# Performance work log

Hardware: AMD Instinct MI355X
Metric: run time of the kernel (lower is better)

The kernel has to match this reference:

```python
import jax, jax.numpy as jnp
import numpy as np


def _graph_conv(src, dst, x, num_nodes, inv_sqrt_out, inv_sqrt_in):
    # DGL GraphConv, norm='both': h = D_in^{-1/2} A D_out^{-1/2} x
    msg = (x * inv_sqrt_out[:, None])[src]                      # [E, F] gather
    agg = jax.ops.segment_sum(msg, dst, num_segments=num_nodes)  # [N, F] scatter-add
    return agg * inv_sqrt_in[:, None]


def setup_inputs() -> dict:
    key = jax.random.key(0)
    ks = jax.random.split(key, 8)
    N, E, IN, H, C = 4096, 131072, 512, 8192, 16
    return {
        "features": jax.random.normal(ks[0], (N, IN), dtype=jnp.float32),
        "W1": jax.random.normal(ks[1], (IN, H), dtype=jnp.float32) * 0.02,
        "b1": jnp.zeros((H,), dtype=jnp.float32),
        "W2": jax.random.normal(ks[2], (H, N), dtype=jnp.float32) * 0.02,
        "Wl": jax.random.normal(ks[3], (N, C), dtype=jnp.float32) * 0.02,
        "bl": jnp.zeros((C,), dtype=jnp.float32),
        "src": jax.random.randint(ks[4], (E,), 0, N, dtype=jnp.int32),
        "dst": jax.random.randint(ks[5], (E,), 0, N, dtype=jnp.int32),
    }


def reference(features, W1, b1, W2, Wl, bl, src, dst):
    N = features.shape[0]
    ones = jnp.ones(src.shape, dtype=features.dtype)
    deg_out = jnp.clip(jax.ops.segment_sum(ones, src, num_segments=N), 1.0)
    deg_in = jnp.clip(jax.ops.segment_sum(ones, dst, num_segments=N), 1.0)
    inv_sqrt_out = jax.lax.rsqrt(deg_out)
    inv_sqrt_in = jax.lax.rsqrt(deg_in)

    # conv1: project then aggregate (math identical to DGL's ordering)
    x = features @ W1 + b1
    x = _graph_conv(src, dst, x, N, inv_sqrt_out, inv_sqrt_in)   # [N, 2N]
    # dropout: identity in inference mode
    # conv2 (weight passed externally, no bias)
    x = x @ W2
    x = _graph_conv(src, dst, x, N, inv_sqrt_out, inv_sqrt_in)   # [N, N]
    x = jax.nn.relu(x)
    x = x @ Wl + bl                                              # [N, C]
    return jax.nn.softmax(x, axis=1)
```

## Files before the change

### kernel.cpp

```cpp
#include <hip/hip_runtime.h>
#include <cstdint>
#include <cstddef>


using bf8   = __attribute__((ext_vector_type(8))) short;
using s4    = __attribute__((ext_vector_type(4))) short;
using f32x4 = __attribute__((ext_vector_type(4))) float;

static __device__ __forceinline__ unsigned short f2bf(float f) {
    union { float f; uint32_t u; } v; v.f = f;
    uint32_t r = (v.u + 0x7FFFu + ((v.u >> 16) & 1u)) >> 16;
    return (unsigned short)r;
}
static __device__ __forceinline__ float bf2f(unsigned short b) {
    union { uint32_t u; float f; } v; v.u = ((uint32_t)b) << 16;
    return v.f;
}

static __device__ __forceinline__ void gload16(const short* g, short* l) {
    __builtin_amdgcn_global_load_lds(
        (const __attribute__((address_space(1))) unsigned int*)g,
        (__attribute__((address_space(3))) unsigned int*)l,
        16, 0, 0);
}


__global__ void k_zero(float* a, float* b, int* c, int n) {
    int i = blockIdx.x * blockDim.x + threadIdx.x;
    if (i < n) { a[i] = 0.f; b[i] = 0.f; c[i] = 0; }
}

__global__ void k_count(const int* __restrict__ src, const int* __restrict__ dst,
                        float* deg_out, float* deg_in, int E) {
    int e = blockIdx.x * blockDim.x + threadIdx.x;
    if (e < E) {
        atomicAdd(&deg_out[src[e]], 1.f);
        atomicAdd(&deg_in[dst[e]], 1.f);
    }
}

__global__ void k_inv(const float* deg_out, const float* deg_in,
                      float* inv_out, float* inv_in, int n) {
    int i = blockIdx.x * blockDim.x + threadIdx.x;
    if (i < n) {
        inv_out[i] = rsqrtf(fmaxf(deg_out[i], 1.f));
        inv_in[i]  = rsqrtf(fmaxf(deg_in[i], 1.f));
    }
}

__global__ void k_scan(const float* __restrict__ deg_in, int* __restrict__ row_off) {
    __shared__ int part[1024];
    const int t = threadIdx.x;
    int v0 = (int)deg_in[t*4+0], v1 = (int)deg_in[t*4+1],
        v2 = (int)deg_in[t*4+2], v3 = (int)deg_in[t*4+3];
    part[t] = v0 + v1 + v2 + v3;
    __syncthreads();
    for (int off = 1; off < 1024; off <<= 1) {
        int x = (t >= off) ? part[t - off] : 0;
        __syncthreads();
        part[t] += x;
        __syncthreads();
    }
    int run = (t == 0) ? 0 : part[t-1];
    row_off[t*4+0] = run; run += v0;
    row_off[t*4+1] = run; run += v1;
    row_off[t*4+2] = run; run += v2;
    row_off[t*4+3] = run; run += v3;
    if (t == 1023) row_off[4096] = run;
}

__global__ void k_fill(const int* __restrict__ src, const int* __restrict__ dst,
                       const int* __restrict__ row_off, int* cursor,
                       int* __restrict__ esrc, int E) {
    int e = blockIdx.x * blockDim.x + threadIdx.x;
    if (e < E) {
        int d = dst[e];
        int p = atomicAdd(&cursor[d], 1);
        esrc[row_off[d] + p] = src[e];
    }
}

__global__ void k_rowsum(const int* __restrict__ row_off, const int* __restrict__ esrc,
                         const float* __restrict__ inv_out, const float* __restrict__ inv_in,
                         float* __restrict__ rowsum) {
    const int node = blockIdx.x, lane = threadIdx.x;
    const int beg = row_off[node], end = row_off[node + 1];
    float s = 0.f;
    for (int p = beg + lane; p < end; p += 64) s += inv_out[esrc[p]];
    #pragma unroll
    for (int off = 32; off; off >>= 1) s += __shfl_down(s, off, 64);
    if (lane == 0) rowsum[node] = s * inv_in[node];
}

__global__ void k_cvt_scale(const float* __restrict__ in, const float* __restrict__ sc,
                            short* __restrict__ out, int n4, int f4) {
    int i = blockIdx.x * blockDim.x + threadIdx.x;
    if (i < n4) {
        const float s = sc[i / f4];
        float4 v = reinterpret_cast<const float4*>(in)[i];
        s4 o;
        o[0] = (short)f2bf(v.x * s); o[1] = (short)f2bf(v.y * s);
        o[2] = (short)f2bf(v.z * s); o[3] = (short)f2bf(v.w * s);
        reinterpret_cast<s4*>(out)[i] = o;
    }
}

__global__ void k_tr2(const float* __restrict__ in, short* __restrict__ out, int R, int C) {
    __shared__ float tile[64][33];
    const int bc = blockIdx.x * 32, br = blockIdx.y * 64;
    const int tx = threadIdx.x, ty = threadIdx.y;
    #pragma unroll
    for (int dy = 0; dy < 64; dy += 8)
        tile[ty + dy][tx] = in[(size_t)(br + ty + dy) * C + bc + tx];
    __syncthreads();
    #pragma unroll
    for (int dy = 0; dy < 32; dy += 8) {
        const int oy = ty + dy;
        ushort2 o;
        o.x = f2bf(tile[tx * 2][oy]);
        o.y = f2bf(tile[tx * 2 + 1][oy]);
        *reinterpret_cast<ushort2*>(&out[(size_t)(bc + oy) * R + br + tx * 2]) = o;
    }
}

template<int EPI>
__global__ __launch_bounds__(512, 2)
void gemm8p(const short* __restrict__ A, const short* __restrict__ Bt,
            short* __restrict__ C,
            const float* __restrict__ bias, const float* __restrict__ rs,
            int M, int N, int K)
{
    constexpr int USZ  = 4096;
    constexpr int BOFF = 4 * USZ;
    constexpr int BUF  = 8 * USZ;
    __shared__ __align__(16) short lds[2 * BUF];
    const int tid  = threadIdx.x;
    const int wid  = tid >> 6, lane = tid & 63;
    const int wm   = wid >> 2;
    const int wn   = wid & 3;
    const int fr   = lane & 15;
    const int kq   = lane >> 4;
    const int nt   = K >> 6;

    const int gx  = gridDim.x;
    const int nwg = gx * gridDim.y;
    int bid = blockIdx.y * gx + blockIdx.x;
    bid = (bid & 7) * (nwg >> 3) + (bid >> 3);
    const int tm = (bid / gx) * 256;
    const int tn = (bid % gx) * 256;

    const int srow = tid >> 3;
    const int scq  = tid & 7;
    const int scs  = scq ^ (srow & 7);
    const short* gA = A  + (size_t)(tm + srow) * K + scs * 8;
    const short* gB = Bt + (size_t)(tn + srow) * K + scs * 8;
    short* const ldst = lds + tid * 8;

    const int cx0 = (0 * 4 + kq) ^ (fr & 7);
    const int cx1 = (1 * 4 + kq) ^ (fr & 7);
    int aoff[8][2], boff[4][2];
    #pragma unroll
    for (int mi = 0; mi < 8; ++mi) {
        const int r = wm * 128 + mi * 16 + fr;
        aoff[mi][0] = r * 64 + cx0 * 8;
        aoff[mi][1] = r * 64 + cx1 * 8;
    }
    #pragma unroll
    for (int n = 0; n < 4; ++n) {
        const int r = wn * 64 + n * 16 + fr;
        boff[n][0] = BOFF + r * 64 + cx0 * 8;
        boff[n][1] = BOFF + r * 64 + cx1 * 8;
    }

    f32x4 acc[8][4];
    #pragma unroll
    for (int mi = 0; mi < 8; ++mi)
        #pragma unroll
        for (int n = 0; n < 4; ++n)
            acc[mi][n] = (f32x4){0.f, 0.f, 0.f, 0.f};

    #pragma unroll
    for (int u = 0; u < 4; ++u) gload16(gA + (size_t)u * 64 * K, ldst + u * USZ);
    #pragma unroll
    for (int v = 0; v < 4; ++v) gload16(gB + (size_t)v * 64 * K, ldst + BOFF + v * USZ);
    #pragma unroll
    for (int u = 0; u < 4; ++u) gload16(gA + (size_t)u * 64 * K + 64, ldst + BUF + u * USZ);
    #pragma unroll
    for (int v = 0; v < 4; ++v) gload16(gB + (size_t)v * 64 * K + 64, ldst + BUF + BOFF + v * USZ);
    asm volatile("s_waitcnt vmcnt(8)" ::: "memory");
    __builtin_amdgcn_sched_barrier(0);
    __builtin_amdgcn_s_barrier();

    for (int t = 0; t < nt; ++t) {
        const int cc = (t & 1) * BUF;
        const bool pf = (t + 2 < nt);
        const size_t kf = (size_t)(t + 2) * 64;

        bf8 a03[4][2], a47[4][2], bg[4][2];

        #pragma unroll
        for (int mi = 0; mi < 4; ++mi)
            #pragma unroll
            for (int s = 0; s < 2; ++s)
                a03[mi][s] = *reinterpret_cast<const bf8*>(lds + cc + aoff[mi][s]);
        #pragma unroll
        for (int n = 0; n < 2; ++n)
            #pragma unroll
            for (int s = 0; s < 2; ++s)
                bg[n][s] = *reinterpret_cast<const bf8*>(lds + cc + boff[n][s]);
        __builtin_amdgcn_s_barrier();
        asm volatile("s_waitcnt lgkmcnt(0)" ::: "memory");
        __builtin_amdgcn_sched_barrier(0);
        __builtin_amdgcn_s_setprio(1);
        #pragma unroll
        for (int mi = 0; mi < 4; ++mi)
            #pragma unroll
            for (int n = 0; n < 2; ++n)
                #pragma unroll
                for (int s = 0; s < 2; ++s)
                    acc[mi][n] = __builtin_amdgcn_mfma_f32_16x16x32_bf16(a03[mi][s], bg[n][s], acc[mi][n], 0, 0, 0);
        __builtin_amdgcn_s_setprio(0);
        __builtin_amdgcn_s_barrier();

        #pragma unroll
        for (int n = 2; n < 4; ++n)
            #pragma unroll
            for (int s = 0; s < 2; ++s)
                bg[n][s] = *reinterpret_cast<const bf8*>(lds + cc + boff[n][s]);
        __builtin_amdgcn_s_barrier();
        asm volatile("s_waitcnt lgkmcnt(0)" ::: "memory");
        __builtin_amdgcn_sched_barrier(0);
        __builtin_amdgcn_s_setprio(1);
        #pragma unroll
        for (int mi = 0; mi < 4; ++mi)
            #pragma unroll
            for (int n = 2; n < 4; ++n)
                #pragma unroll
                for (int s = 0; s < 2; ++s)
                    acc[mi][n] = __builtin_amdgcn_mfma_f32_16x16x32_bf16(a03[mi][s], bg[n][s], acc[mi][n], 0, 0, 0);
        __builtin_amdgcn_s_setprio(0);
        __builtin_amdgcn_s_barrier();

        #pragma unroll
        for (int mi = 0; mi < 4; ++mi)
            #pragma unroll
            for (int s = 0; s < 2; ++s)
                a47[mi][s] = *reinterpret_cast<const bf8*>(lds + cc + aoff[4 + mi][s]);
        if (pf) {
            #pragma unroll
            for (int v = 0; v < 4; ++v)
                gload16(gB + (size_t)v * 64 * K + kf, ldst + cc + BOFF + v * USZ);
        }
        __builtin_amdgcn_s_barrier();
        asm volatile("s_waitcnt lgkmcnt(0)" ::: "memory");
        __builtin_amdgcn_sched_barrier(0);
        __builtin_amdgcn_s_setprio(1);
        #pragma unroll
        for (int mi = 0; mi < 4; ++mi)
            #pragma unroll
            for (int n = 0; n < 2; ++n)
                #pragma unroll
                for (int s = 0; s < 2; ++s)
                    acc[4 + mi][n] = __builtin_amdgcn_mfma_f32_16x16x32_bf16(a47[mi][s], bg[n][s], acc[4 + mi][n], 0, 0, 0);
        __builtin_amdgcn_s_setprio(0);
        __builtin_amdgcn_s_barrier();

        if (pf) {
            #pragma unroll
            for (int u = 0; u < 4; ++u)
                gload16(gA + (size_t)u * 64 * K + kf, ldst + cc + u * USZ);
        }
        __builtin_amdgcn_s_setprio(1);
        #pragma unroll
        for (int mi = 0; mi < 4; ++mi)
            #pragma unroll
            for (int n = 2; n < 4; ++n)
                #pragma unroll
                for (int s = 0; s < 2; ++s)
                    acc[4 + mi][n] = __builtin_amdgcn_mfma_f32_16x16x32_bf16(a47[mi][s], bg[n][s], acc[4 + mi][n], 0, 0, 0);
        __builtin_amdgcn_s_setprio(0);
        if (pf) {
            asm volatile("s_waitcnt vmcnt(8)" ::: "memory");
        } else if (t + 2 == nt) {
            asm volatile("s_waitcnt vmcnt(0)" ::: "memory");
        }
        __builtin_amdgcn_sched_barrier(0);
        __builtin_amdgcn_s_barrier();
    }

    const int rb = kq * 4;
    #pragma unroll
    for (int mi = 0; mi < 8; ++mi) {
        #pragma unroll
        for (int n = 0; n < 4; ++n) {
            const int col = tn + wn * 64 + n * 16 + fr;
            const float bcol = (EPI == 1) ? bias[col] : 0.f;
            #pragma unroll
            for (int j = 0; j < 4; ++j) {
                const int row = tm + wm * 128 + mi * 16 + rb + j;
                float v = acc[mi][n][j];
                if (EPI == 1) v += rs[row] * bcol;
                else          v *= rs[row];
                C[(size_t)row * N + col] = (short)f2bf(v);
            }
        }
    }
}

template<int RELU>
__global__ __launch_bounds__(64)
void agg_strip(const short* __restrict__ X, short* __restrict__ Y,
               const int* __restrict__ row_off, const int* __restrict__ esrc,
               const float* __restrict__ inv_in, int F)
{
    const int node = blockIdx.y;
    const int c0 = blockIdx.x * 512 + threadIdx.x * 8;
    float acc[8];
    #pragma unroll
    for (int j = 0; j < 8; ++j) acc[j] = 0.f;

    const int beg = row_off[node], end = row_off[node + 1];
    int p = beg;
    for (; p + 3 < end; p += 4) {
        const int s0 = esrc[p], s1 = esrc[p + 1], s2 = esrc[p + 2], s3 = esrc[p + 3];
        bf8 x0 = *reinterpret_cast<const bf8*>(X + (size_t)s0 * F + c0);
        bf8 x1 = *reinterpret_cast<const bf8*>(X + (size_t)s1 * F + c0);
        bf8 x2 = *reinterpret_cast<const bf8*>(X + (size_t)s2 * F + c0);
        bf8 x3 = *reinterpret_cast<const bf8*>(X + (size_t)s3 * F + c0);
        #pragma unroll
        for (int j = 0; j < 8; ++j)
            acc[j] += (bf2f((unsigned short)x0[j]) + bf2f((unsigned short)x1[j]))
                    + (bf2f((unsigned short)x2[j]) + bf2f((unsigned short)x3[j]));
    }
    for (; p < end; ++p) {
        const int s0 = esrc[p];
        bf8 x0 = *reinterpret_cast<const bf8*>(X + (size_t)s0 * F + c0);
        #pragma unroll
        for (int j = 0; j < 8; ++j) acc[j] += bf2f((unsigned short)x0[j]);
    }
    const float sc = inv_in[node];
    bf8 o;
    #pragma unroll
    for (int j = 0; j < 8; ++j) {
        float v = acc[j] * sc;
        if (RELU) v = fmaxf(v, 0.f);
        o[j] = (short)f2bf(v);
    }
    *reinterpret_cast<bf8*>(Y + (size_t)node * F + c0) = o;
}

__global__ __launch_bounds__(256)
void k_head(const short* __restrict__ H, const float* __restrict__ Wl,
            const float* __restrict__ bl, float* __restrict__ out)
{
    const int row = blockIdx.x;
    const int tid = threadIdx.x;
    float acc[16];
    #pragma unroll
    for (int c = 0; c < 16; ++c) acc[c] = 0.f;

    for (int k = tid; k < 4096; k += 256) {
        const float x = bf2f((unsigned short)H[(size_t)row * 4096 + k]);
        const float4* w = reinterpret_cast<const float4*>(Wl + (size_t)k * 16);
        float4 w0 = w[0], w1 = w[1], w2 = w[2], w3 = w[3];
        acc[0]  += x * w0.x; acc[1]  += x * w0.y; acc[2]  += x * w0.z; acc[3]  += x * w0.w;
        acc[4]  += x * w1.x; acc[5]  += x * w1.y; acc[6]  += x * w1.z; acc[7]  += x * w1.w;
        acc[8]  += x * w2.x; acc[9]  += x * w2.y; acc[10] += x * w2.z; acc[11] += x * w2.w;
        acc[12] += x * w3.x; acc[13] += x * w3.y; acc[14] += x * w3.z; acc[15] += x * w3.w;
    }
    #pragma unroll
    for (int c = 0; c < 16; ++c)
        for (int off = 32; off; off >>= 1)
            acc[c] += __shfl_down(acc[c], off, 64);

    __shared__ float sm[16][4];
    const int wid = tid >> 6, lane = tid & 63;
    if (lane == 0) {
        #pragma unroll
        for (int c = 0; c < 16; ++c) sm[c][wid] = acc[c];
    }
    __syncthreads();
    if (tid < 16) {
        float l = sm[tid][0] + sm[tid][1] + sm[tid][2] + sm[tid][3] + bl[tid];
        float mx = l;
        #pragma unroll
        for (int off = 1; off < 16; off <<= 1) mx = fmaxf(mx, __shfl_xor(mx, off, 16));
        float e = expf(l - mx);
        float s = e;
        #pragma unroll
        for (int off = 1; off < 16; off <<= 1) s += __shfl_xor(s, off, 16);
        out[(size_t)row * 16 + tid] = e / s;
    }
}


extern "C" void kernel_launch(void* const* d_in, const int* in_sizes, int n_in,
                              void* d_out, int out_size, void* d_ws, size_t ws_size,
                              hipStream_t stream)
{
    const float* features = (const float*)d_in[0];
    const float* W1       = (const float*)d_in[1];
    const float* b1       = (const float*)d_in[2];
    const float* W2       = (const float*)d_in[3];
    const float* Wl       = (const float*)d_in[4];
    const float* bl       = (const float*)d_in[5];
    const int*   src      = (const int*)d_in[6];
    const int*   dst      = (const int*)d_in[7];
    float* out = (float*)d_out;

    const int N = 4096, IN = 512, H = 8192;
    const int E = in_sizes[6];

    char* ws = (char*)d_ws;
    size_t o = 0;
    auto alloc = [&](size_t bytes) -> char* {
        char* p = ws + o;
        o = (o + bytes + 255) & ~(size_t)255;
        return p;
    };
    short* W2t   = (short*)alloc((size_t)N * H * 2);
    short* h1    = (short*)alloc((size_t)N * H * 2);
    short* x2s   = (short*)alloc((size_t)N * N * 2);
    short* featb = (short*)alloc((size_t)N * IN * 2);
    short* aggF  = (short*)alloc((size_t)N * IN * 2);
    short* W1t   = (short*)alloc((size_t)H * IN * 2);
    float* deg_out = (float*)alloc(N * 4);
    float* deg_in  = (float*)alloc(N * 4);
    float* inv_out = (float*)alloc(N * 4);
    float* inv_in  = (float*)alloc(N * 4);
    float* rowsum  = (float*)alloc(N * 4);
    int*   cursor  = (int*)alloc(N * 4);
    int*   row_off = (int*)alloc((N + 1) * 4);
    int*   esrc    = (int*)alloc((size_t)E * 4);
    short* h2 = h1;

    k_zero <<<(N + 255) / 256, 256, 0, stream>>>(deg_out, deg_in, cursor, N);
    k_count<<<(E + 255) / 256, 256, 0, stream>>>(src, dst, deg_out, deg_in, E);
    k_inv  <<<(N + 255) / 256, 256, 0, stream>>>(deg_out, deg_in, inv_out, inv_in, N);
    k_scan <<<1, 1024, 0, stream>>>(deg_in, row_off);
    k_fill <<<(E + 255) / 256, 256, 0, stream>>>(src, dst, row_off, cursor, esrc, E);
    k_rowsum<<<N, 64, 0, stream>>>(row_off, esrc, inv_out, inv_in, rowsum);

    k_cvt_scale<<<(N * IN / 4 + 255) / 256, 256, 0, stream>>>(features, inv_out, featb,
                                                              N * IN / 4, IN / 4);
    k_tr2<<<dim3(H / 32, IN / 64), dim3(32, 8), 0, stream>>>(W1, W1t, IN, H);
    k_tr2<<<dim3(N / 32, H / 64), dim3(32, 8), 0, stream>>>(W2, W2t, H, N);

    agg_strip<0><<<dim3(1, N), 64, 0, stream>>>(featb, aggF, row_off, esrc, inv_in, IN);
    gemm8p<1><<<dim3(H / 256, N / 256), 512, 0, stream>>>(aggF, W1t, h1, b1, rowsum, N, H, IN);

    gemm8p<2><<<dim3(N / 256, N / 256), 512, 0, stream>>>(h1, W2t, x2s, nullptr, inv_out, N, N, H);
    agg_strip<1><<<dim3(N / 512, N), 64, 0, stream>>>(x2s, h2, row_off, esrc, inv_in, N);

    k_head<<<N, 256, 0, stream>>>(h2, Wl, bl, out);
}
```

Before: 476.0 us.

## Simplify GEMM main loop to single-phase load/compute with fewer barriers

Replaces the four-phase ping-pong main loop, which interleaved LDS reads, MFMA quadrants, setprio and global prefetches across several barriers, with one simpler loop per K-tile. Each iteration waits on vmcnt, takes one barrier, reads all A/B fragments per k-slice, issues all 32 MFMAs, then takes a second barrier and prefetches the tile two steps ahead. This cuts barrier count and scheduling complexity. In exchange it loses the fine-grained overlap of LDS reads and global loads with MFMA work, and the s_setprio wave prioritisation.

```diff
diff --git a/kernel.cpp b/kernel.cpp
--- a/kernel.cpp
+++ b/kernel.cpp
@@ -187,105 +187,43 @@
     for (int u = 0; u < 4; ++u) gload16(gA + (size_t)u * 64 * K + 64, ldst + BUF + u * USZ);
     #pragma unroll
     for (int v = 0; v < 4; ++v) gload16(gB + (size_t)v * 64 * K + 64, ldst + BUF + BOFF + v * USZ);
-    asm volatile("s_waitcnt vmcnt(8)" ::: "memory");
-    __builtin_amdgcn_sched_barrier(0);
-    __builtin_amdgcn_s_barrier();
 
     for (int t = 0; t < nt; ++t) {
         const int cc = (t & 1) * BUF;
-        const bool pf = (t + 2 < nt);
-        const size_t kf = (size_t)(t + 2) * 64;
-
-        bf8 a03[4][2], a47[4][2], bg[4][2];
-
-        #pragma unroll
-        for (int mi = 0; mi < 4; ++mi)
-            #pragma unroll
-            for (int s = 0; s < 2; ++s)
-                a03[mi][s] = *reinterpret_cast<const bf8*>(lds + cc + aoff[mi][s]);
-        #pragma unroll
-        for (int n = 0; n < 2; ++n)
-            #pragma unroll
-            for (int s = 0; s < 2; ++s)
-                bg[n][s] = *reinterpret_cast<const bf8*>(lds + cc + boff[n][s]);
+
+        if (t + 1 < nt) { asm volatile("s_waitcnt vmcnt(8)" ::: "memory"); }
+        else            { asm volatile("s_waitcnt vmcnt(0)" ::: "memory"); }
+        __builtin_amdgcn_sched_barrier(0);
         __builtin_amdgcn_s_barrier();
+
+        #pragma unroll
+        for (int s = 0; s < 2; ++s) {
+            bf8 b[4], a[8];
+            #pragma unroll
+            for (int n = 0; n < 4; ++n)
+                b[n] = *reinterpret_cast<const bf8*>(lds + cc + boff[n][s]);
+            #pragma unroll
+            for (int mi = 0; mi < 8; ++mi)
+                a[mi] = *reinterpret_cast<const bf8*>(lds + cc + aoff[mi][s]);
+            #pragma unroll
+            for (int mi = 0; mi < 8; ++mi)
+                #pragma unroll
+                for (int n = 0; n < 4; ++n)
+                    acc[mi][n] = __builtin_amdgcn_mfma_f32_16x16x32_bf16(a[mi], b[n], acc[mi][n], 0, 0, 0);
+        }
+
         asm volatile("s_waitcnt lgkmcnt(0)" ::: "memory");
         __builtin_amdgcn_sched_barrier(0);
-        __builtin_amdgcn_s_setprio(1);
-        #pragma unroll
-        for (int mi = 0; mi < 4; ++mi)
-            #pragma unroll
-            for (int n = 0; n < 2; ++n)
-                #pragma unroll
-                for (int s = 0; s < 2; ++s)
-                    acc[mi][n] = __builtin_amdgcn_mfma_f32_16x16x32_bf16(a03[mi][s], bg[n][s], acc[mi][n], 0, 0, 0);
-        __builtin_amdgcn_s_setprio(0);
         __builtin_amdgcn_s_barrier();
-
-        #pragma unroll
-        for (int n = 2; n < 4; ++n)
-            #pragma unroll
-            for (int s = 0; s < 2; ++s)
-                bg[n][s] = *reinterpret_cast<const bf8*>(lds + cc + boff[n][s]);
-        __builtin_amdgcn_s_barrier();
-        asm volatile("s_waitcnt lgkmcnt(0)" ::: "memory");
-        __builtin_amdgcn_sched_barrier(0);
-        __builtin_amdgcn_s_setprio(1);
-        #pragma unroll
-        for (int mi = 0; mi < 4; ++mi)
-            #pragma unroll
-            for (int n = 2; n < 4; ++n)
-                #pragma unroll
-                for (int s = 0; s < 2; ++s)
-                    acc[mi][n] = __builtin_amdgcn_mfma_f32_16x16x32_bf16(a03[mi][s], bg[n][s], acc[mi][n], 0, 0, 0);
-        __builtin_amdgcn_s_setprio(0);
-        __builtin_amdgcn_s_barrier();
-
-        #pragma unroll
-        for (int mi = 0; mi < 4; ++mi)
-            #pragma unroll
-            for (int s = 0; s < 2; ++s)
-                a47[mi][s] = *reinterpret_cast<const bf8*>(lds + cc + aoff[4 + mi][s]);
-        if (pf) {
+        if (t + 2 < nt) {
+            const size_t kf = (size_t)(t + 2) * 64;
+            #pragma unroll
+            for (int u = 0; u < 4; ++u)
+                gload16(gA + (size_t)u * 64 * K + kf, ldst + cc + u * USZ);
             #pragma unroll
             for (int v = 0; v < 4; ++v)
                 gload16(gB + (size_t)v * 64 * K + kf, ldst + cc + BOFF + v * USZ);
         }
-        __builtin_amdgcn_s_barrier();
-        asm volatile("s_waitcnt lgkmcnt(0)" ::: "memory");
-        __builtin_amdgcn_sched_barrier(0);
-        __builtin_amdgcn_s_setprio(1);
-        #pragma unroll
-        for (int mi = 0; mi < 4; ++mi)
-            #pragma unroll
-            for (int n = 0; n < 2; ++n)
-                #pragma unroll
-                for (int s = 0; s < 2; ++s)
-                    acc[4 + mi][n] = __builtin_amdgcn_mfma_f32_16x16x32_bf16(a47[mi][s], bg[n][s], acc[4 + mi][n], 0, 0, 0);
-        __builtin_amdgcn_s_setprio(0);
-        __builtin_amdgcn_s_barrier();
-
-        if (pf) {
-            #pragma unroll
-            for (int u = 0; u < 4; ++u)
-                gload16(gA + (size_t)u * 64 * K + kf, ldst + cc + u * USZ);
-        }
-        __builtin_amdgcn_s_setprio(1);
-        #pragma unroll
-        for (int mi = 0; mi < 4; ++mi)
-            #pragma unroll
-            for (int n = 2; n < 4; ++n)
-                #pragma unroll
-                for (int s = 0; s < 2; ++s)
-                    acc[4 + mi][n] = __builtin_amdgcn_mfma_f32_16x16x32_bf16(a47[mi][s], bg[n][s], acc[4 + mi][n], 0, 0, 0);
-        __builtin_amdgcn_s_setprio(0);
-        if (pf) {
-            asm volatile("s_waitcnt vmcnt(8)" ::: "memory");
-        } else if (t + 2 == nt) {
-            asm volatile("s_waitcnt vmcnt(0)" ::: "memory");
-        }
-        __builtin_amdgcn_sched_barrier(0);
-        __builtin_amdgcn_s_barrier();
     }
 
     const int rb = kq * 4;
```

After: 482.1 us. No clear change (+1.3%).

## Software-pipeline LDS fragment loads across K iterations in GEMM main loop

Applied to the files above, without the earlier changes.

Restructures the GEMM main loop so fragments for the next K-tile (aL, bL) are read from LDS during the current iteration's MFMA phases, rather than at the start of each iteration. It also removes the explicit lgkmcnt(0) waits and sched_barriers and splits the A global prefetch into two halves issued at different phases. The goal is to hide LDS read latency behind MFMAs and spread global-to-LDS traffic more evenly. In exchange it uses more registers, and correctness now depends on the reworked barrier and vmcnt ordering, since buffers are reused while next-tile reads are in flight.

```diff
diff --git a/kernel.cpp b/kernel.cpp
--- a/kernel.cpp
+++ b/kernel.cpp
@@ -179,6 +179,8 @@
         for (int n = 0; n < 4; ++n)
             acc[mi][n] = (f32x4){0.f, 0.f, 0.f, 0.f};
 
+    bf8 aL[4][2], aH[4][2], bL[2][2], bH[2][2];
+
     #pragma unroll
     for (int u = 0; u < 4; ++u) gload16(gA + (size_t)u * 64 * K, ldst + u * USZ);
     #pragma unroll
@@ -191,26 +193,49 @@
     __builtin_amdgcn_sched_barrier(0);
     __builtin_amdgcn_s_barrier();
 
+    #pragma unroll
+    for (int mi = 0; mi < 4; ++mi)
+        #pragma unroll
+        for (int s = 0; s < 2; ++s)
+            aL[mi][s] = *reinterpret_cast<const bf8*>(lds + aoff[mi][s]);
+    #pragma unroll
+    for (int n = 0; n < 2; ++n)
+        #pragma unroll
+        for (int s = 0; s < 2; ++s)
+            bL[n][s] = *reinterpret_cast<const bf8*>(lds + boff[n][s]);
+
     for (int t = 0; t < nt; ++t) {
         const int cc = (t & 1) * BUF;
+        const int cn = cc ^ BUF;
         const bool pf = (t + 2 < nt);
+        const bool nx = (t + 1 < nt);
         const size_t kf = (size_t)(t + 2) * 64;
 
-        bf8 a03[4][2], a47[4][2], bg[4][2];
-
+        if (!nx) { asm volatile("s_waitcnt vmcnt(0)" ::: "memory"); }
+
+        #pragma unroll
+        for (int n = 0; n < 2; ++n)
+            #pragma unroll
+            for (int s = 0; s < 2; ++s)
+                bH[n][s] = *reinterpret_cast<const bf8*>(lds + cc + boff[2 + n][s]);
+        __builtin_amdgcn_s_barrier();
+        __builtin_amdgcn_s_setprio(1);
         #pragma unroll
         for (int mi = 0; mi < 4; ++mi)
             #pragma unroll
+            for (int n = 0; n < 2; ++n)
+                #pragma unroll
+                for (int s = 0; s < 2; ++s)
+                    acc[mi][n] = __builtin_amdgcn_mfma_f32_16x16x32_bf16(aL[mi][s], bL[n][s], acc[mi][n], 0, 0, 0);
+        __builtin_amdgcn_s_setprio(0);
+        __builtin_amdgcn_s_barrier();
+
+        #pragma unroll
+        for (int mi = 0; mi < 4; ++mi)
+            #pragma unroll
             for (int s = 0; s < 2; ++s)
-                a03[mi][s] = *reinterpret_cast<const bf8*>(lds + cc + aoff[mi][s]);
-        #pragma unroll
-        for (int n = 0; n < 2; ++n)
-            #pragma unroll
-            for (int s = 0; s < 2; ++s)
-                bg[n][s] = *reinterpret_cast<const bf8*>(lds + cc + boff[n][s]);
-        __builtin_amdgcn_s_barrier();
-        asm volatile("s_waitcnt lgkmcnt(0)" ::: "memory");
-        __builtin_amdgcn_sched_barrier(0);
+                aH[mi][s] = *reinterpret_cast<const bf8*>(lds + cc + aoff[4 + mi][s]);
+        __builtin_amdgcn_s_barrier();
         __builtin_amdgcn_s_setprio(1);
         #pragma unroll
         for (int mi = 0; mi < 4; ++mi)
@@ -218,73 +243,60 @@
             for (int n = 0; n < 2; ++n)
                 #pragma unroll
                 for (int s = 0; s < 2; ++s)
-                    acc[mi][n] = __builtin_amdgcn_mfma_f32_16x16x32_bf16(a03[mi][s], bg[n][s], acc[mi][n], 0, 0, 0);
+                    acc[mi][2 + n] = __builtin_amdgcn_mfma_f32_16x16x32_bf16(aL[mi][s], bH[n][s], acc[mi][2 + n], 0, 0, 0);
         __builtin_amdgcn_s_setprio(0);
         __builtin_amdgcn_s_barrier();
 
-        #pragma unroll
-        for (int n = 2; n < 4; ++n)
-            #pragma unroll
-            for (int s = 0; s < 2; ++s)
-                bg[n][s] = *reinterpret_cast<const bf8*>(lds + cc + boff[n][s]);
-        __builtin_amdgcn_s_barrier();
-        asm volatile("s_waitcnt lgkmcnt(0)" ::: "memory");
-        __builtin_amdgcn_sched_barrier(0);
-        __builtin_amdgcn_s_setprio(1);
-        #pragma unroll
-        for (int mi = 0; mi < 4; ++mi)
-            #pragma unroll
-            for (int n = 2; n < 4; ++n)
-                #pragma unroll
-                for (int s = 0; s < 2; ++s)
-                    acc[mi][n] = __builtin_amdgcn_mfma_f32_16x16x32_bf16(a03[mi][s], bg[n][s], acc[mi][n], 0, 0, 0);
-        __builtin_amdgcn_s_setprio(0);
-        __builtin_amdgcn_s_barrier();
-
-        #pragma unroll
-        for (int mi = 0; mi < 4; ++mi)
-            #pragma unroll
-            for (int s = 0; s < 2; ++s)
-                a47[mi][s] = *reinterpret_cast<const bf8*>(lds + cc + aoff[4 + mi][s]);
         if (pf) {
             #pragma unroll
             for (int v = 0; v < 4; ++v)
                 gload16(gB + (size_t)v * 64 * K + kf, ldst + cc + BOFF + v * USZ);
-        }
-        __builtin_amdgcn_s_barrier();
-        asm volatile("s_waitcnt lgkmcnt(0)" ::: "memory");
-        __builtin_amdgcn_sched_barrier(0);
-        __builtin_amdgcn_s_setprio(1);
-        #pragma unroll
-        for (int mi = 0; mi < 4; ++mi)
-            #pragma unroll
-            for (int n = 0; n < 2; ++n)
-                #pragma unroll
-                for (int s = 0; s < 2; ++s)
-                    acc[4 + mi][n] = __builtin_amdgcn_mfma_f32_16x16x32_bf16(a47[mi][s], bg[n][s], acc[4 + mi][n], 0, 0, 0);
-        __builtin_amdgcn_s_setprio(0);
-        __builtin_amdgcn_s_barrier();
-
-        if (pf) {
-            #pragma unroll
-            for (int u = 0; u < 4; ++u)
-                gload16(gA + (size_t)u * 64 * K + kf, ldst + cc + u * USZ);
-        }
-        __builtin_amdgcn_s_setprio(1);
-        #pragma unroll
-        for (int mi = 0; mi < 4; ++mi)
-            #pragma unroll
-            for (int n = 2; n < 4; ++n)
-                #pragma unroll
-                for (int s = 0; s < 2; ++s)
-                    acc[4 + mi][n] = __builtin_amdgcn_mfma_f32_16x16x32_bf16(a47[mi][s], bg[n][s], acc[4 + mi][n], 0, 0, 0);
-        __builtin_amdgcn_s_setprio(0);
-        if (pf) {
-            asm volatile("s_waitcnt vmcnt(8)" ::: "memory");
-        } else if (t + 2 == nt) {
+            gload16(gA + (size_t)0 * 64 * K + kf, ldst + cc + 0 * USZ);
+            gload16(gA + (size_t)2 * 64 * K + kf, ldst + cc + 2 * USZ);
+            asm volatile("s_waitcnt vmcnt(6)" ::: "memory");
+        } else {
             asm volatile("s_waitcnt vmcnt(0)" ::: "memory");
         }
-        __builtin_amdgcn_sched_barrier(0);
+        if (nx) {
+            #pragma unroll
+            for (int mi = 0; mi < 4; ++mi)
+                #pragma unroll
+                for (int s = 0; s < 2; ++s)
+                    aL[mi][s] = *reinterpret_cast<const bf8*>(lds + cn + aoff[mi][s]);
+        }
+        __builtin_amdgcn_s_barrier();
+        __builtin_amdgcn_s_setprio(1);
+        #pragma unroll
+        for (int mi = 0; mi < 4; ++mi)
+            #pragma unroll
+            for (int n = 0; n < 2; ++n)
+                #pragma unroll
+                for (int s = 0; s < 2; ++s)
+                    acc[4 + mi][n] = __builtin_amdgcn_mfma_f32_16x16x32_bf16(aH[mi][s], bL[n][s], acc[4 + mi][n], 0, 0, 0);
+        __builtin_amdgcn_s_setprio(0);
+        __builtin_amdgcn_s_barrier();
+
+        if (pf) {
+            gload16(gA + (size_t)1 * 64 * K + kf, ldst + cc + 1 * USZ);
+            gload16(gA + (size_t)3 * 64 * K + kf, ldst + cc + 3 * USZ);
+        }
+        if (nx) {
+            #pragma unroll
+            for (int n = 0; n < 2; ++n)
+                #pragma unroll
+                for (int s = 0; s < 2; ++s)
+                    bL[n][s] = *reinterpret_cast<const bf8*>(lds + cn + boff[n][s]);
+        }
+        __builtin_amdgcn_s_barrier();
+        __builtin_amdgcn_s_setprio(1);
+        #pragma unroll
+        for (int mi = 0; mi < 4; ++mi)
+            #pragma unroll
+            for (int n = 0; n < 2; ++n)
+                #pragma unroll
+                for (int s = 0; s < 2; ++s)
+                    acc[4 + mi][2 + n] = __builtin_amdgcn_mfma_f32_16x16x32_bf16(aH[mi][s], bH[n][s], acc[4 + mi][2 + n], 0, 0, 0);
+        __builtin_amdgcn_s_setprio(0);
         __builtin_amdgcn_s_barrier();
     }
 
```

After: 493.6 us. 1.04x slower.
